# Kernel optimization log

Hardware: AMD Instinct MI355X
Metric: run time of the kernel (lower is better)

Reference implementation:

```python
import jax, jax.numpy as jnp
import numpy as np

C = 64   # input_channels
H = 128  # hidden_channels


def setup_inputs() -> dict:
    key = jax.random.key(0)
    ks = jax.random.split(key, 13)
    s = lambda k, shape, fan_in: jax.random.uniform(k, shape, jnp.float32, -1.0, 1.0) / np.sqrt(fan_in)
    return {
        "x": jax.random.normal(ks[0], (2, 512, C), jnp.float32),
        "Wa": s(ks[1], (C, H), C),  "ba": s(ks[2], (H,), C),
        "Wb": s(ks[3], (H, H), H), "bb": s(ks[4], (H,), H),
        "Wc1": s(ks[5], (H, H), H), "bc1": s(ks[6], (H,), H),
        "Wc2": s(ks[7], (H, H), H), "bc2": s(ks[8], (H,), H),
        "Wc3": s(ks[9], (H, H), H), "bc3": s(ks[10], (H,), H),
        "Wo": s(ks[11], (H, 1), H), "bo": s(ks[12], (1,), H),
    }


def reference(x, Wa, ba, Wb, bb, Wc1, bc1, Wc2, bc2, Wc3, bc3, Wo, bo):
    B, N, _ = x.shape
    # node MLP
    h = jax.nn.relu(jnp.einsum("bnc,ch->bnh", x, Wa) + ba)
    h = jax.nn.relu(jnp.einsum("bnh,hk->bnk", h, Wb) + bb)
    # pairwise difference: diff[b,i,j] = h[b,j] - h[b,i]  (matches x_a - x_b)
    d = h[:, None, :, :] - h[:, :, None, :]  # [B,N,N,H]
    e = jax.nn.relu(jnp.einsum("bijh,hk->bijk", d, Wc1) + bc1)
    e = jax.nn.relu(jnp.einsum("bijh,hk->bijk", e, Wc2) + bc2)
    e = jax.nn.relu(jnp.einsum("bijh,hk->bijk", e, Wc3) + bc3)
    out = jnp.einsum("bijh,ho->bijo", e, Wo) + bo  # [B,N,N,1]
    return out[..., 0]  # [B,N,N]
```

## Files before the change

kernel.cpp:

```cpp
#include <hip/hip_runtime.h>


typedef _Float16 half_t;
typedef __attribute__((ext_vector_type(2))) _Float16 f16x2;
typedef __attribute__((ext_vector_type(8))) _Float16 f16x8;
typedef __attribute__((ext_vector_type(4))) float f32x4;


__global__ __launch_bounds__(256) void prep_kernel(
    const float* __restrict__ x, const float* __restrict__ Wa, const float* __restrict__ ba,
    const float* __restrict__ Wb, const float* __restrict__ bb, const float* __restrict__ Wc1,
    const float* __restrict__ bc1, const float* __restrict__ Wc2, const float* __restrict__ Wc3,
    half_t* __restrict__ gh, half_t* __restrict__ gbh,
    half_t* __restrict__ W2T, half_t* __restrict__ W3T)
{
  const int t = threadIdx.x;
  if (blockIdx.x >= 256) {
    const int bid = blockIdx.x - 256;
    const int layer = bid >> 3, nt = bid & 7;
    const int ks = t >> 6, L = t & 63, q = L >> 4, cc = L & 15;
    const float* src = layer ? Wc3 : Wc2;
    half_t* dst = layer ? W3T : W2T;
    f16x8 v;
    #pragma unroll
    for (int e = 0; e < 8; e++)
      v[e] = (half_t)src[(32 * ks + 8 * q + e) * 128 + 16 * nt + cc];
    *(f16x8*)(dst + (nt * 4 + ks) * 512 + L * 8) = v;
    return;
  }
  __shared__ float sx[64 * 6];
  __shared__ float sh1[128 * 6];
  __shared__ float sh2[128 * 6];
  const int n0 = blockIdx.x * 4;
  const int col = t & 127, hf = t >> 7;

  sx[(t & 63) * 6 + (t >> 6)] = x[(n0 + (t >> 6)) * 64 + (t & 63)];
  __syncthreads();

  float a0 = ba[col], a1 = a0;
  #pragma unroll
  for (int cc = 0; cc < 64; cc++) {
    const float wv = Wa[cc * 128 + col];
    const float2 xv = *(const float2*)(sx + cc * 6 + hf * 2);
    a0 = fmaf(xv.x, wv, a0); a1 = fmaf(xv.y, wv, a1);
  }
  *(float2*)(sh1 + col * 6 + hf * 2) = make_float2(fmaxf(a0, 0.f), fmaxf(a1, 0.f));
  __syncthreads();

  float b0 = bb[col], b1 = b0;
  #pragma unroll
  for (int k = 0; k < 128; k++) {
    const float wv = Wb[k * 128 + col];
    const float2 hv = *(const float2*)(sh1 + k * 6 + hf * 2);
    b0 = fmaf(hv.x, wv, b0); b1 = fmaf(hv.y, wv, b1);
  }
  *(float2*)(sh2 + col * 6 + hf * 2) = make_float2(fmaxf(b0, 0.f), fmaxf(b1, 0.f));
  __syncthreads();

  float c0 = 0.f, c1 = 0.f;
  #pragma unroll
  for (int k = 0; k < 128; k++) {
    const float wv = Wc1[k * 128 + col];
    const float2 hv = *(const float2*)(sh2 + k * 6 + hf * 2);
    c0 = fmaf(hv.x, wv, c0); c1 = fmaf(hv.y, wv, c1);
  }
  const float bv = bc1[col];
  const int r0 = n0 + hf * 2;
  gh [(r0 + 0) * 128 + col] = (half_t)c0;
  gh [(r0 + 1) * 128 + col] = (half_t)c1;
  gbh[(r0 + 0) * 128 + col] = (half_t)(c0 + bv);
  gbh[(r0 + 1) * 128 + col] = (half_t)(c1 + bv);
}

static __device__ inline f16x8 relu_sub8(f16x8 a, f16x8 b) {
  f16x8 d = a - b;
  const f16x8 z = {};
  return __builtin_elementwise_max(d, z);
}

__global__ __launch_bounds__(512, 2)
void edge_kernel(
    const half_t* __restrict__ gh, const half_t* __restrict__ gbh,
    const half_t* __restrict__ W2T, const half_t* __restrict__ W3T,
    const float* __restrict__ bc2, const float* __restrict__ bc3,
    const float* __restrict__ Wo, const float* __restrict__ bo,
    float* __restrict__ out)
{
  __shared__ __align__(16) half_t sW2[16384];
  __shared__ __align__(16) half_t sW3[16384];
  __shared__ __align__(16) float  sBf[384];
  __shared__ __align__(16) half_t sE[8 * 4096];

  const int t = threadIdx.x, lane = t & 63, w = t >> 6;
  const int c = lane & 15, q = lane >> 4;
  const int bid = blockIdx.x;
  const int b = bid >> 8, jh = (bid >> 7) & 1, ic = bid & 127;
  const int i0 = ic * 4;
  const int j0w = jh * 256 + w * 32;

  #pragma unroll
  for (int k = 0; k < 4; k++) {
    const int off = (k * 512 + t) * 8;
    *(f16x8*)(sW2 + off) = *(const f16x8*)(W2T + off);
    *(f16x8*)(sW3 + off) = *(const f16x8*)(W3T + off);
  }
  if (t < 384) sBf[t] = (t < 128) ? bc2[t] : ((t < 256) ? bc3[t - 128] : Wo[t - 256]);
  __syncthreads();

  half_t* sEw = sE + w * 4096;
  const float bo0 = bo[0];
  const int packoff = ((q >> 1) * 16 + c) * 8 + (q & 1) * 4;
  const int rdoff = lane * 8;

  f16x8 gj[4][2];
  #pragma unroll
  for (int ks = 0; ks < 4; ks++)
    #pragma unroll
    for (int jt = 0; jt < 2; jt++)
      gj[ks][jt] = *(const f16x8*)(gbh + (size_t)(b * 512 + j0w + jt * 16 + c) * 128 + ks * 32 + q * 8);

  #pragma unroll 1
  for (int u = 0; u < 4; u++) {
    const int i = i0 + u;

    f16x8 e1[4][2];
    {
      f16x8 gih[4];
      #pragma unroll
      for (int ks = 0; ks < 4; ks++)
        gih[ks] = *(const f16x8*)(gh + (size_t)(b * 512 + i) * 128 + ks * 32 + q * 8);
      #pragma unroll
      for (int ks = 0; ks < 4; ks++)
        #pragma unroll
        for (int jt = 0; jt < 2; jt++)
          e1[ks][jt] = relu_sub8(gj[ks][jt], gih[ks]);
    }

    #pragma unroll
    for (int nt = 0; nt < 8; nt++) {
      f16x8 wf[4];
      #pragma unroll
      for (int ks = 0; ks < 4; ks++)
        wf[ks] = *(const f16x8*)(sW2 + nt * 2048 + ks * 512 + rdoff);
      const f32x4 b2 = *(const f32x4*)(sBf + nt * 16 + q * 4);
      f32x4 acc[2] = {b2, b2};
      __builtin_amdgcn_s_setprio(1);
      #pragma unroll
      for (int ks = 0; ks < 4; ks++)
        #pragma unroll
        for (int jt = 0; jt < 2; jt++)
          acc[jt] = __builtin_amdgcn_mfma_f32_16x16x32_f16(wf[ks], e1[ks][jt], acc[jt], 0, 0, 0);
      __builtin_amdgcn_s_setprio(0);
      const int po = ((nt >> 1) * 512) + packoff + (nt & 1) * 256;
      #pragma unroll
      for (int jt = 0; jt < 2; jt++) {
        const f32x4 v = acc[jt];
        f16x2 h01, h23;
        h01[0] = (half_t)fmaxf(v[0], 0.f); h01[1] = (half_t)fmaxf(v[1], 0.f);
        h23[0] = (half_t)fmaxf(v[2], 0.f); h23[1] = (half_t)fmaxf(v[3], 0.f);
        uint2 uv;
        uv.x = __builtin_bit_cast(unsigned int, h01);
        uv.y = __builtin_bit_cast(unsigned int, h23);
        *(uint2*)(sEw + jt * 2048 + po) = uv;
      }
    }

    f16x8 be[4][2];
    #pragma unroll
    for (int ks3 = 0; ks3 < 4; ks3++)
      #pragma unroll
      for (int jt = 0; jt < 2; jt++)
        be[ks3][jt] = *(const f16x8*)(sEw + (jt * 4 + ks3) * 512 + rdoff);

    float p[2] = {0.f, 0.f};
    #pragma unroll
    for (int nt = 0; nt < 8; nt++) {
      f16x8 wf[4];
      #pragma unroll
      for (int ks3 = 0; ks3 < 4; ks3++)
        wf[ks3] = *(const f16x8*)(sW3 + nt * 2048 + ks3 * 512 + rdoff);
      const f32x4 b3 = *(const f32x4*)(sBf + 128 + nt * 16 + q * 4);
      f32x4 acc[2] = {b3, b3};
      __builtin_amdgcn_s_setprio(1);
      #pragma unroll
      for (int ks3 = 0; ks3 < 4; ks3++)
        #pragma unroll
        for (int jt = 0; jt < 2; jt++)
          acc[jt] = __builtin_amdgcn_mfma_f32_16x16x32_f16(wf[ks3], be[ks3][jt], acc[jt], 0, 0, 0);
      __builtin_amdgcn_s_setprio(0);
      const f32x4 wo = *(const f32x4*)(sBf + 256 + nt * 16 + q * 4);
      #pragma unroll
      for (int jt = 0; jt < 2; jt++)
        #pragma unroll
        for (int r = 0; r < 4; r++)
          p[jt] = fmaf(fmaxf(acc[jt][r], 0.f), wo[r], p[jt]);
    }

    #pragma unroll
    for (int jt = 0; jt < 2; jt++) {
      p[jt] += __shfl_xor(p[jt], 16, 64);
      p[jt] += __shfl_xor(p[jt], 32, 64);
    }
    if (q == 0) {
      const size_t base = ((size_t)(b * 512 + i)) * 512 + j0w;
      #pragma unroll
      for (int jt = 0; jt < 2; jt++)
        out[base + jt * 16 + c] = p[jt] + bo0;
    }
  }
}

extern "C" void kernel_launch(void* const* d_in, const int* in_sizes, int n_in,
                              void* d_out, int out_size, void* d_ws, size_t ws_size,
                              hipStream_t stream)
{
  const float* x   = (const float*)d_in[0];
  const float* Wa  = (const float*)d_in[1];
  const float* ba  = (const float*)d_in[2];
  const float* Wb  = (const float*)d_in[3];
  const float* bb  = (const float*)d_in[4];
  const float* Wc1 = (const float*)d_in[5];
  const float* bc1 = (const float*)d_in[6];
  const float* Wc2 = (const float*)d_in[7];
  const float* bc2 = (const float*)d_in[8];
  const float* Wc3 = (const float*)d_in[9];
  const float* bc3 = (const float*)d_in[10];
  const float* Wo  = (const float*)d_in[11];
  const float* bo  = (const float*)d_in[12];
  float* out = (float*)d_out;

  char* ws = (char*)d_ws;
  half_t* gh  = (half_t*)ws;
  half_t* gbh = (half_t*)(ws + 262144);
  half_t* W2T = (half_t*)(ws + 524288);
  half_t* W3T = (half_t*)(ws + 557056);

  prep_kernel<<<272, 256, 0, stream>>>(x, Wa, ba, Wb, bb, Wc1, bc1, Wc2, Wc3,
                                       gh, gbh, W2T, W3T);
  edge_kernel<<<512, 512, 0, stream>>>(gh, gbh, W2T, W3T, bc2, bc3, Wo, bo, out);
}
```

Before: 118.7 us.

## Halve nodes per prep block, stagger edge waves, move bias adds after MFMA

The prep kernel now handles two nodes per block instead of four, so it launches twice as many blocks for more parallelism on the small node MLP. In the edge kernel the upper four waves sleep briefly after setup to stagger their start against the lower four. MFMA accumulators now start at zero and the layer-2 and layer-3 biases are added in the epilogue instead of being preloaded. The extra prep blocks each redo weight loads, and the sleep adds a fixed delay to half the waves.

```diff
diff --git a/kernel.cpp b/kernel.cpp
--- a/kernel.cpp
+++ b/kernel.cpp
@@ -15,8 +15,8 @@
     half_t* __restrict__ W2T, half_t* __restrict__ W3T)
 {
   const int t = threadIdx.x;
-  if (blockIdx.x >= 256) {
-    const int bid = blockIdx.x - 256;
+  if (blockIdx.x >= 512) {
+    const int bid = blockIdx.x - 512;
     const int layer = bid >> 3, nt = bid & 7;
     const int ks = t >> 6, L = t & 63, q = L >> 4, cc = L & 15;
     const float* src = layer ? Wc3 : Wc2;
@@ -28,48 +28,36 @@
     *(f16x8*)(dst + (nt * 4 + ks) * 512 + L * 8) = v;
     return;
   }
-  __shared__ float sx[64 * 6];
-  __shared__ float sh1[128 * 6];
-  __shared__ float sh2[128 * 6];
-  const int n0 = blockIdx.x * 4;
+  __shared__ float sx[128];
+  __shared__ float sh1[256];
+  __shared__ float sh2[256];
+  const int n0 = blockIdx.x * 2;
   const int col = t & 127, hf = t >> 7;
 
-  sx[(t & 63) * 6 + (t >> 6)] = x[(n0 + (t >> 6)) * 64 + (t & 63)];
-  __syncthreads();
-
-  float a0 = ba[col], a1 = a0;
-  #pragma unroll
-  for (int cc = 0; cc < 64; cc++) {
-    const float wv = Wa[cc * 128 + col];
-    const float2 xv = *(const float2*)(sx + cc * 6 + hf * 2);
-    a0 = fmaf(xv.x, wv, a0); a1 = fmaf(xv.y, wv, a1);
-  }
-  *(float2*)(sh1 + col * 6 + hf * 2) = make_float2(fmaxf(a0, 0.f), fmaxf(a1, 0.f));
-  __syncthreads();
-
-  float b0 = bb[col], b1 = b0;
-  #pragma unroll
-  for (int k = 0; k < 128; k++) {
-    const float wv = Wb[k * 128 + col];
-    const float2 hv = *(const float2*)(sh1 + k * 6 + hf * 2);
-    b0 = fmaf(hv.x, wv, b0); b1 = fmaf(hv.y, wv, b1);
-  }
-  *(float2*)(sh2 + col * 6 + hf * 2) = make_float2(fmaxf(b0, 0.f), fmaxf(b1, 0.f));
-  __syncthreads();
-
-  float c0 = 0.f, c1 = 0.f;
-  #pragma unroll
-  for (int k = 0; k < 128; k++) {
-    const float wv = Wc1[k * 128 + col];
-    const float2 hv = *(const float2*)(sh2 + k * 6 + hf * 2);
-    c0 = fmaf(hv.x, wv, c0); c1 = fmaf(hv.y, wv, c1);
-  }
-  const float bv = bc1[col];
-  const int r0 = n0 + hf * 2;
-  gh [(r0 + 0) * 128 + col] = (half_t)c0;
-  gh [(r0 + 1) * 128 + col] = (half_t)c1;
-  gbh[(r0 + 0) * 128 + col] = (half_t)(c0 + bv);
-  gbh[(r0 + 1) * 128 + col] = (half_t)(c1 + bv);
+  if (t < 128) sx[t] = x[(n0 + (t >> 6)) * 64 + (t & 63)];
+  __syncthreads();
+
+  float a = ba[col];
+  #pragma unroll
+  for (int cc = 0; cc < 64; cc++)
+    a = fmaf(sx[hf * 64 + cc], Wa[cc * 128 + col], a);
+  sh1[hf * 128 + col] = fmaxf(a, 0.f);
+  __syncthreads();
+
+  float bacc = bb[col];
+  #pragma unroll
+  for (int k = 0; k < 128; k++)
+    bacc = fmaf(sh1[hf * 128 + k], Wb[k * 128 + col], bacc);
+  sh2[hf * 128 + col] = fmaxf(bacc, 0.f);
+  __syncthreads();
+
+  float cacc = 0.f;
+  #pragma unroll
+  for (int k = 0; k < 128; k++)
+    cacc = fmaf(sh2[hf * 128 + k], Wc1[k * 128 + col], cacc);
+  const int r = n0 + hf;
+  gh [r * 128 + col] = (half_t)cacc;
+  gbh[r * 128 + col] = (half_t)(cacc + bc1[col]);
 }
 
 static __device__ inline f16x8 relu_sub8(f16x8 a, f16x8 b) {
@@ -107,7 +95,8 @@
   if (t < 384) sBf[t] = (t < 128) ? bc2[t] : ((t < 256) ? bc3[t - 128] : Wo[t - 256]);
   __syncthreads();
 
-  half_t* sEw = sE + w * 4096;
+  if (w >= 4) __builtin_amdgcn_s_sleep(99);
+
   const float bo0 = bo[0];
   const int packoff = ((q >> 1) * 16 + c) * 8 + (q & 1) * 4;
   const int rdoff = lane * 8;
@@ -119,6 +108,8 @@
     for (int jt = 0; jt < 2; jt++)
       gj[ks][jt] = *(const f16x8*)(gbh + (size_t)(b * 512 + j0w + jt * 16 + c) * 128 + ks * 32 + q * 8);
 
+  half_t* sEw = sE + w * 4096;
+
   #pragma unroll 1
   for (int u = 0; u < 4; u++) {
     const int i = i0 + u;
@@ -138,12 +129,12 @@
 
     #pragma unroll
     for (int nt = 0; nt < 8; nt++) {
+      const f32x4 b2 = *(const f32x4*)(sBf + nt * 16 + q * 4);
       f16x8 wf[4];
       #pragma unroll
       for (int ks = 0; ks < 4; ks++)
         wf[ks] = *(const f16x8*)(sW2 + nt * 2048 + ks * 512 + rdoff);
-      const f32x4 b2 = *(const f32x4*)(sBf + nt * 16 + q * 4);
-      f32x4 acc[2] = {b2, b2};
+      f32x4 acc[2] = {};
       __builtin_amdgcn_s_setprio(1);
       #pragma unroll
       for (int ks = 0; ks < 4; ks++)
@@ -156,8 +147,8 @@
       for (int jt = 0; jt < 2; jt++) {
         const f32x4 v = acc[jt];
         f16x2 h01, h23;
-        h01[0] = (half_t)fmaxf(v[0], 0.f); h01[1] = (half_t)fmaxf(v[1], 0.f);
-        h23[0] = (half_t)fmaxf(v[2], 0.f); h23[1] = (half_t)fmaxf(v[3], 0.f);
+        h01[0] = (half_t)fmaxf(v[0] + b2[0], 0.f); h01[1] = (half_t)fmaxf(v[1] + b2[1], 0.f);
+        h23[0] = (half_t)fmaxf(v[2] + b2[2], 0.f); h23[1] = (half_t)fmaxf(v[3] + b2[3], 0.f);
         uint2 uv;
         uv.x = __builtin_bit_cast(unsigned int, h01);
         uv.y = __builtin_bit_cast(unsigned int, h23);
@@ -175,12 +166,13 @@
     float p[2] = {0.f, 0.f};
     #pragma unroll
     for (int nt = 0; nt < 8; nt++) {
+      const f32x4 b3 = *(const f32x4*)(sBf + 128 + nt * 16 + q * 4);
+      const f32x4 wo = *(const f32x4*)(sBf + 256 + nt * 16 + q * 4);
       f16x8 wf[4];
       #pragma unroll
       for (int ks3 = 0; ks3 < 4; ks3++)
         wf[ks3] = *(const f16x8*)(sW3 + nt * 2048 + ks3 * 512 + rdoff);
-      const f32x4 b3 = *(const f32x4*)(sBf + 128 + nt * 16 + q * 4);
-      f32x4 acc[2] = {b3, b3};
+      f32x4 acc[2] = {};
       __builtin_amdgcn_s_setprio(1);
       #pragma unroll
       for (int ks3 = 0; ks3 < 4; ks3++)
@@ -188,12 +180,11 @@
         for (int jt = 0; jt < 2; jt++)
           acc[jt] = __builtin_amdgcn_mfma_f32_16x16x32_f16(wf[ks3], be[ks3][jt], acc[jt], 0, 0, 0);
       __builtin_amdgcn_s_setprio(0);
-      const f32x4 wo = *(const f32x4*)(sBf + 256 + nt * 16 + q * 4);
       #pragma unroll
       for (int jt = 0; jt < 2; jt++)
         #pragma unroll
         for (int r = 0; r < 4; r++)
-          p[jt] = fmaf(fmaxf(acc[jt][r], 0.f), wo[r], p[jt]);
+          p[jt] = fmaf(fmaxf(acc[jt][r] + b3[r], 0.f), wo[r], p[jt]);
     }
 
     #pragma unroll
@@ -235,7 +226,7 @@
   half_t* W2T = (half_t*)(ws + 524288);
   half_t* W3T = (half_t*)(ws + 557056);
 
-  prep_kernel<<<272, 256, 0, stream>>>(x, Wa, ba, Wb, bb, Wc1, bc1, Wc2, Wc3,
+  prep_kernel<<<528, 256, 0, stream>>>(x, Wa, ba, Wb, bb, Wc1, bc1, Wc2, Wc3,
                                        gh, gbh, W2T, W3T);
   edge_kernel<<<512, 512, 0, stream>>>(gh, gbh, W2T, W3T, bc2, bc3, Wo, bo, out);
 }
```

Measured after the change: 123.1 us. 1.04x slower.
